# Optimization experiments

Measured on AMD Instinct MI355X. Metric: run time of the kernel, lower is better.

The kernel has to match this reference:

```python
import jax, jax.numpy as jnp
import numpy as np

B = 262144
STEPS = 15            # Program.steps = var(15)
SPEED = 5.0           # Program.straight_speed
TRAJ_IDX = np.array([10, 1, 2, 3, 4, 5, 6, 7, 8, 17])
FEAT_IDX = np.array([1, 2, 3, 4, 9, 17])


def setup_inputs() -> dict:
    key = jax.random.key(0)
    ks = jax.random.split(key, 9)
    x = jax.random.normal(ks[0], (B, 18), dtype=jnp.float32)
    x = x.at[:, 0].set(0.0)  # loop counter i starts at 0 -> exactly 15 iterations
    return {
        "x": x,
        "c1w": jax.random.normal(ks[1], (2,), jnp.float32) * 0.5,
        "c1b": jax.random.normal(ks[2], (1,), jnp.float32) * 0.1,
        "c2w": jax.random.normal(ks[3], (2,), jnp.float32) * 0.5,
        "c2b": jax.random.normal(ks[4], (1,), jnp.float32) * 0.1,
        "l1w": jax.random.normal(ks[5], (4, 32), jnp.float32) * 0.3,
        "l1b": jax.random.normal(ks[6], (32,), jnp.float32) * 0.1,
        "l2w": jax.random.normal(ks[7], (32, 5), jnp.float32) * 0.3,
        "l2b": jax.random.normal(ks[8], (5,), jnp.float32) * 0.1,
    }


def _classifier(feat, c1w, c1b, c2w, c2b, l1w, l1b, l2w, l2b):
    # feat: [B,6] -> conv1d(k=2): [B,5] -> conv1d(k=2): [B,4] -> 32 -> 5, sigmoid
    h = jax.nn.relu(c1w[0] * feat[:, :-1] + c1w[1] * feat[:, 1:] + c1b)
    h = jax.nn.relu(c2w[0] * h[:, :-1] + c2w[1] * h[:, 1:] + c2b)
    h = jax.nn.relu(h @ l1w + l1b)
    return jax.nn.sigmoid(h @ l2w + l2b)  # [B,5]


def _distance(s):
    return (s[:, 1] - s[:, 3]) ** 2 + (s[:, 2] - s[:, 4]) ** 2


def _program(x, c1w, c1b, c2w, c2b, l1w, l1b, l2w, l2b):
    s = x.at[:, 10].set(_distance(x))          # initial assign_distance
    traj0 = s[:, TRAJ_IDX]                      # initial trajectory_update

    def step(s, _):
        # assign_branch_probability
        p = _classifier(s[:, FEAT_IDX], c1w, c1b, c2w, c2b, l1w, l1b, l2w, l2b)
        s = (s.at[:, 5].set(p[:, 0]).at[:, 6].set(p[:, 1]).at[:, 7].set(p[:, 2])
              .at[:, 8].set(p[:, 3]).at[:, 17].set(p[:, 4]))
        p5, p6, p7, p8 = p[:, 0], p[:, 1], p[:, 2], p[:, 3]
        # assign_comparison_block: pairwise diffs a..f at indices 11..16
        a, b, c = p6 - p5, p7 - p5, p8 - p5
        d, e, f = p7 - p6, p8 - p6, p8 - p7
        s = (s.at[:, 11].set(a).at[:, 12].set(b).at[:, 13].set(c)
              .at[:, 14].set(d).at[:, 15].set(e).at[:, 16].set(f))
        # ifelse_argmax_ITE: nested compare against comparison_bar=0.0
        dx_c = jnp.where(c <= 0.0, 0.0, SPEED);  st_c = jnp.where(c <= 0.0, 0.0, 3.0)   # cruise vs right
        dx_f = jnp.where(f <= 0.0, 0.0, SPEED);  st_f = jnp.where(f <= 0.0, 2.0, 3.0)   # straight vs right
        dx_e = jnp.where(e <= 0.0, -SPEED, SPEED); st_e = jnp.where(e <= 0.0, 1.0, 3.0)  # left vs right
        dx_b = jnp.where(b <= 0.0, dx_c, dx_f);  st_b = jnp.where(b <= 0.0, st_c, st_f)
        dx_d = jnp.where(d <= 0.0, dx_e, dx_f);  st_d = jnp.where(d <= 0.0, st_e, st_f)
        dx   = jnp.where(a <= 0.0, dx_b, dx_d);  st   = jnp.where(a <= 0.0, st_b, st_d)
        s = s.at[:, 1].add(dx).at[:, 9].set(st)
        # assign_y1, assign_x2, assign_update_i, assign_distance
        s = s.at[:, 2].add(SPEED).at[:, 3].add(SPEED).at[:, 0].add(1.0)
        s = s.at[:, 10].set(_distance(s))
        return s, s[:, TRAJ_IDX]

    s, recs = jax.lax.scan(step, s, None, length=STEPS)
    traj = jnp.concatenate([traj0[:, None, :], jnp.moveaxis(recs, 0, 1)], axis=1)  # [B,16,10]
    return jnp.concatenate([s, traj.reshape(s.shape[0], -1)], axis=1)  # [B, 18+160]


def reference(x, c1w, c1b, c2w, c2b, l1w, l1b, l2w, l2b):
    return _program(x, c1w, c1b, c2w, c2b, l1w, l1b, l2w, l2b)
```

## Files before the change

kernel.cpp:

```cpp
#include <hip/hip_runtime.h>


constexpr int kB     = 262144;
constexpr int kSteps = 15;

__device__ __forceinline__ float relu_(float v) { return fmaxf(v, 0.0f); }
__device__ __forceinline__ float sigmoid_(float v) {
    return __builtin_amdgcn_rcpf(1.0f + __expf(-v));
}

__global__ __launch_bounds__(256) void Program_4578435138231_kernel(
    const float* __restrict__ x,
    const float* __restrict__ c1w, const float* __restrict__ c1b,
    const float* __restrict__ c2w, const float* __restrict__ c2b,
    const float* __restrict__ l1w, const float* __restrict__ l1b,
    const float* __restrict__ l2w, const float* __restrict__ l2b,
    float* __restrict__ out)
{
    const int i = blockIdx.x * 256 + threadIdx.x;
    if (i >= kB) return;

    const float2* xr = reinterpret_cast<const float2*>(x + (size_t)i * 18);
    float s[18];
    #pragma unroll
    for (int j = 0; j < 9; ++j) {
        float2 v = xr[j];
        s[2 * j]     = v.x;
        s[2 * j + 1] = v.y;
    }

    const float cw10 = c1w[0], cw11 = c1w[1], cb1 = c1b[0];
    const float cw20 = c2w[0], cw21 = c2w[1], cb2 = c2b[0];

    {
        float dA = s[1] - s[3], dB = s[2] - s[4];
        s[10] = dA * dA + dB * dB;
    }

    float* orow = out + (size_t)i * 178;

    {
        float2* tr = reinterpret_cast<float2*>(orow + 18);
        tr[0] = make_float2(s[10], s[1]);
        tr[1] = make_float2(s[2],  s[3]);
        tr[2] = make_float2(s[4],  s[5]);
        tr[3] = make_float2(s[6],  s[7]);
        tr[4] = make_float2(s[8],  s[17]);
    }

    #pragma unroll 1
    for (int t = 0; t < kSteps; ++t) {
        float f0 = s[1], f1 = s[2], f2 = s[3], f3 = s[4], f4 = s[9], f5 = s[17];
        float h10 = relu_(cw10 * f0 + cw11 * f1 + cb1);
        float h11 = relu_(cw10 * f1 + cw11 * f2 + cb1);
        float h12 = relu_(cw10 * f2 + cw11 * f3 + cb1);
        float h13 = relu_(cw10 * f3 + cw11 * f4 + cb1);
        float h14 = relu_(cw10 * f4 + cw11 * f5 + cb1);
        float g0 = relu_(cw20 * h10 + cw21 * h11 + cb2);
        float g1 = relu_(cw20 * h11 + cw21 * h12 + cb2);
        float g2 = relu_(cw20 * h12 + cw21 * h13 + cb2);
        float g3 = relu_(cw20 * h13 + cw21 * h14 + cb2);

        float p0 = l2b[0], p1 = l2b[1], p2 = l2b[2], p3 = l2b[3], p4 = l2b[4];
        #pragma unroll
        for (int k = 0; k < 32; ++k) {
            float h = g0 * l1w[k] + g1 * l1w[32 + k] + g2 * l1w[64 + k]
                    + g3 * l1w[96 + k] + l1b[k];
            h = relu_(h);
            p0 += h * l2w[5 * k + 0];
            p1 += h * l2w[5 * k + 1];
            p2 += h * l2w[5 * k + 2];
            p3 += h * l2w[5 * k + 3];
            p4 += h * l2w[5 * k + 4];
        }
        p0 = sigmoid_(p0); p1 = sigmoid_(p1); p2 = sigmoid_(p2);
        p3 = sigmoid_(p3); p4 = sigmoid_(p4);

        s[5] = p0; s[6] = p1; s[7] = p2; s[8] = p3; s[17] = p4;
        float a = p1 - p0, b = p2 - p0, c = p3 - p0;
        float d = p2 - p1, e = p3 - p1, f = p3 - p2;
        s[11] = a; s[12] = b; s[13] = c; s[14] = d; s[15] = e; s[16] = f;

        float dx_c = (c <= 0.f) ? 0.f  : 5.f,  st_c = (c <= 0.f) ? 0.f : 3.f;
        float dx_f = (f <= 0.f) ? 0.f  : 5.f,  st_f = (f <= 0.f) ? 2.f : 3.f;
        float dx_e = (e <= 0.f) ? -5.f : 5.f,  st_e = (e <= 0.f) ? 1.f : 3.f;
        float dx_b = (b <= 0.f) ? dx_c : dx_f, st_b = (b <= 0.f) ? st_c : st_f;
        float dx_d = (d <= 0.f) ? dx_e : dx_f, st_d = (d <= 0.f) ? st_e : st_f;
        float dx   = (a <= 0.f) ? dx_b : dx_d, st   = (a <= 0.f) ? st_b : st_d;

        s[1] += dx; s[9] = st;
        s[2] += 5.f; s[3] += 5.f; s[0] += 1.f;
        float dA = s[1] - s[3], dB = s[2] - s[4];
        s[10] = dA * dA + dB * dB;

        float2* tr = reinterpret_cast<float2*>(orow + 18 + 10 * (t + 1));
        tr[0] = make_float2(s[10], s[1]);
        tr[1] = make_float2(s[2],  s[3]);
        tr[2] = make_float2(s[4],  s[5]);
        tr[3] = make_float2(s[6],  s[7]);
        tr[4] = make_float2(s[8],  s[17]);
    }

    float2* os = reinterpret_cast<float2*>(orow);
    #pragma unroll
    for (int j = 0; j < 9; ++j) os[j] = make_float2(s[2 * j], s[2 * j + 1]);
}

extern "C" void kernel_launch(void* const* d_in, const int* in_sizes, int n_in,
                              void* d_out, int out_size, void* d_ws, size_t ws_size,
                              hipStream_t stream) {
    const float* x   = (const float*)d_in[0];
    const float* c1w = (const float*)d_in[1];
    const float* c1b = (const float*)d_in[2];
    const float* c2w = (const float*)d_in[3];
    const float* c2b = (const float*)d_in[4];
    const float* l1w = (const float*)d_in[5];
    const float* l1b = (const float*)d_in[6];
    const float* l2w = (const float*)d_in[7];
    const float* l2b = (const float*)d_in[8];
    float* out = (float*)d_out;

    Program_4578435138231_kernel<<<kB / 256, 256, 0, stream>>>(
        x, c1w, c1b, c2w, c2b, l1w, l1b, l2w, l2b, out);
}
```

Before: 296.8 us.

## Stage trajectory records in LDS as packed bf16 for coalesced output stores

Each thread now writes its trajectory records and final state into shared memory as packed bf16 pairs. The block then cooperatively writes them to global memory so consecutive lanes store consecutive float2 words, replacing the per-thread strided stores. The block size drops to 64 to keep the LDS buffer small, and the step loop is split into two flush phases. The trade-off is that all outputs lose precision to bf16 rounding, and extra barriers and LDS traffic are added.

```diff
diff --git a/kernel.cpp b/kernel.cpp
--- a/kernel.cpp
+++ b/kernel.cpp
@@ -1,15 +1,21 @@
 #include <hip/hip_runtime.h>
 
 
-constexpr int kB     = 262144;
-constexpr int kSteps = 15;
+constexpr int kB = 262144;
 
 __device__ __forceinline__ float relu_(float v) { return fmaxf(v, 0.0f); }
 __device__ __forceinline__ float sigmoid_(float v) {
     return __builtin_amdgcn_rcpf(1.0f + __expf(-v));
 }
+__device__ __forceinline__ unsigned bf1(float a) {
+    unsigned u = __float_as_uint(a);
+    return (u + 0x7FFFu + ((u >> 16) & 1u)) >> 16;
+}
+__device__ __forceinline__ unsigned pkbf(float lo, float hi) {
+    return bf1(lo) | (bf1(hi) << 16);
+}
 
-__global__ __launch_bounds__(256) void Program_4578435138231_kernel(
+__global__ __launch_bounds__(64) void Program_4578435138231_kernel(
     const float* __restrict__ x,
     const float* __restrict__ c1w, const float* __restrict__ c1b,
     const float* __restrict__ c2w, const float* __restrict__ c2b,
@@ -17,16 +23,17 @@
     const float* __restrict__ l2w, const float* __restrict__ l2b,
     float* __restrict__ out)
 {
-    const int i = blockIdx.x * 256 + threadIdx.x;
-    if (i >= kB) return;
+    __shared__ unsigned lds[64 * 41];
+    const int tid  = threadIdx.x;
+    const int row0 = blockIdx.x * 64;
+    const int row  = row0 + tid;
 
-    const float2* xr = reinterpret_cast<const float2*>(x + (size_t)i * 18);
+    const float2* xr = reinterpret_cast<const float2*>(x + (size_t)row * 18);
     float s[18];
     #pragma unroll
     for (int j = 0; j < 9; ++j) {
         float2 v = xr[j];
-        s[2 * j]     = v.x;
-        s[2 * j + 1] = v.y;
+        s[2 * j] = v.x; s[2 * j + 1] = v.y;
     }
 
     const float cw10 = c1w[0], cw11 = c1w[1], cb1 = c1b[0];
@@ -37,25 +44,21 @@
         s[10] = dA * dA + dB * dB;
     }
 
-    float* orow = out + (size_t)i * 178;
+    auto write_rec = [&](int col) {
+        const int base = tid * 41 + col;
+        lds[base + 0] = pkbf(s[10], s[1]);
+        lds[base + 1] = pkbf(s[2],  s[3]);
+        lds[base + 2] = pkbf(s[4],  s[5]);
+        lds[base + 3] = pkbf(s[6],  s[7]);
+        lds[base + 4] = pkbf(s[8],  s[17]);
+    };
 
-    {
-        float2* tr = reinterpret_cast<float2*>(orow + 18);
-        tr[0] = make_float2(s[10], s[1]);
-        tr[1] = make_float2(s[2],  s[3]);
-        tr[2] = make_float2(s[4],  s[5]);
-        tr[3] = make_float2(s[6],  s[7]);
-        tr[4] = make_float2(s[8],  s[17]);
-    }
-
-    #pragma unroll 1
-    for (int t = 0; t < kSteps; ++t) {
-        float f0 = s[1], f1 = s[2], f2 = s[3], f3 = s[4], f4 = s[9], f5 = s[17];
-        float h10 = relu_(cw10 * f0 + cw11 * f1 + cb1);
-        float h11 = relu_(cw10 * f1 + cw11 * f2 + cb1);
-        float h12 = relu_(cw10 * f2 + cw11 * f3 + cb1);
-        float h13 = relu_(cw10 * f3 + cw11 * f4 + cb1);
-        float h14 = relu_(cw10 * f4 + cw11 * f5 + cb1);
+    auto step = [&]() {
+        float h10 = relu_(cw10 * s[1] + cw11 * s[2]  + cb1);
+        float h11 = relu_(cw10 * s[2] + cw11 * s[3]  + cb1);
+        float h12 = relu_(cw10 * s[3] + cw11 * s[4]  + cb1);
+        float h13 = relu_(cw10 * s[4] + cw11 * s[9]  + cb1);
+        float h14 = relu_(cw10 * s[9] + cw11 * s[17] + cb1);
         float g0 = relu_(cw20 * h10 + cw21 * h11 + cb2);
         float g1 = relu_(cw20 * h11 + cw21 * h12 + cb2);
         float g2 = relu_(cw20 * h12 + cw21 * h13 + cb2);
@@ -92,18 +95,55 @@
         s[2] += 5.f; s[3] += 5.f; s[0] += 1.f;
         float dA = s[1] - s[3], dB = s[2] - s[4];
         s[10] = dA * dA + dB * dB;
+    };
 
-        float2* tr = reinterpret_cast<float2*>(orow + 18 + 10 * (t + 1));
-        tr[0] = make_float2(s[10], s[1]);
-        tr[1] = make_float2(s[2],  s[3]);
-        tr[2] = make_float2(s[4],  s[5]);
-        tr[3] = make_float2(s[6],  s[7]);
-        tr[4] = make_float2(s[8],  s[17]);
+    float2* out2 = reinterpret_cast<float2*>(out);
+
+    auto flush40 = [&](int outD0) {
+        __syncthreads();
+        #pragma unroll
+        for (int k = 0; k < 40; ++k) {
+            int g = tid + 64 * k;
+            int r = g / 40, c = g - r * 40;
+            unsigned v = lds[r * 41 + c];
+            out2[(size_t)(row0 + r) * 89 + outD0 + c] =
+                make_float2(__uint_as_float(v << 16),
+                            __uint_as_float(v & 0xFFFF0000u));
+        }
+        __syncthreads();
+    };
+
+    write_rec(0);
+    #pragma unroll 1
+    for (int t = 0; t < 7; ++t) { step(); write_rec(5 * (t + 1)); }
+    flush40(9);
+
+    #pragma unroll 1
+    for (int t = 7; t < 15; ++t) { step(); write_rec(5 * (t - 7)); }
+    flush40(49);
+
+    {
+        const int base = tid * 41;
+        lds[base + 0] = pkbf(s[0],  s[1]);
+        lds[base + 1] = pkbf(s[2],  s[3]);
+        lds[base + 2] = pkbf(s[4],  s[5]);
+        lds[base + 3] = pkbf(s[6],  s[7]);
+        lds[base + 4] = pkbf(s[8],  s[9]);
+        lds[base + 5] = pkbf(s[10], s[11]);
+        lds[base + 6] = pkbf(s[12], s[13]);
+        lds[base + 7] = pkbf(s[14], s[15]);
+        lds[base + 8] = pkbf(s[16], s[17]);
+        __syncthreads();
+        #pragma unroll
+        for (int k = 0; k < 9; ++k) {
+            int g = tid + 64 * k;
+            int r = g / 9, c = g - r * 9;
+            unsigned v = lds[r * 41 + c];
+            out2[(size_t)(row0 + r) * 89 + c] =
+                make_float2(__uint_as_float(v << 16),
+                            __uint_as_float(v & 0xFFFF0000u));
+        }
     }
-
-    float2* os = reinterpret_cast<float2*>(orow);
-    #pragma unroll
-    for (int j = 0; j < 9; ++j) os[j] = make_float2(s[2 * j], s[2 * j + 1]);
 }
 
 extern "C" void kernel_launch(void* const* d_in, const int* in_sizes, int n_in,
@@ -120,6 +160,6 @@
     const float* l2b = (const float*)d_in[8];
     float* out = (float*)d_out;
 
-    Program_4578435138231_kernel<<<kB / 256, 256, 0, stream>>>(
+    Program_4578435138231_kernel<<<kB / 64, 64, 0, stream>>>(
         x, c1w, c1b, c2w, c2b, l1w, l1b, l2w, l2b, out);
 }
```

Result: slower. 308.8 us (+4.0%).
